# Kernel tuning notes

Hardware: AMD Instinct MI355X
Metric: run time of the kernel (lower is better)

Reference implementation:

```python
import jax, jax.numpy as jnp
import numpy as np

PARENTS = [-1, 0, 0, 0, 1, 2, 3, 4, 5, 6, 7, 8, 9, 9, 9, 12, 13, 14, 16, 17, 18, 19, 20, 21]
K = 24          # num_joints (SMPL kinematic tree)
BONE = 12       # 3x3 rotation (9) + 3 rel offset
FEAT = 64       # local_feature_size
B = 65536       # batch
NIN = BONE + 1 + FEAT  # 77: bone_transform(13) concat parent feature(64)


def setup_inputs() -> dict:
    key = jax.random.key(0)
    ks = jax.random.split(key, 6)
    pose = jax.random.normal(ks[0], (B, K, 3, 3), jnp.float32)
    rel_joints = jax.random.normal(ks[1], (B, K, 3), jnp.float32)
    # proj_bone_prior: Linear(K*BONE -> FEAT)
    Wp = jax.random.normal(ks[2], (K * BONE, FEAT), jnp.float32) * 0.05
    bp = jnp.zeros((FEAT,), jnp.float32)
    # per-joint BoneMLP: Linear(NIN->NIN), ReLU, Linear(NIN->FEAT), ReLU (stacked over K)
    W1 = jax.random.normal(ks[3], (K, NIN, NIN), jnp.float32) * 0.05
    b1 = jnp.zeros((K, NIN), jnp.float32)
    W2 = jax.random.normal(ks[4], (K, NIN, FEAT), jnp.float32) * 0.05
    b2 = jnp.zeros((K, FEAT), jnp.float32)
    return {"pose": pose, "rel_joints": rel_joints, "Wp": Wp, "bp": bp,
            "W1": W1, "b1": b1, "W2": W2, "b2": b2}


def reference(pose, rel_joints, Wp, bp, W1, b1, W2, b2):
    Bn, Kn = rel_joints.shape[0], rel_joints.shape[1]
    bone_lengths = jnp.linalg.norm(rel_joints, axis=-1, keepdims=True)          # B,K,1
    bone_features = jnp.concatenate([pose.reshape(Bn, Kn, 9), rel_joints], -1)  # B,K,12
    root_bone_prior = bone_features.reshape(Bn, -1) @ Wp + bp                   # B,FEAT
    bone_transforms = jnp.concatenate([bone_features, bone_lengths], -1)        # B,K,13
    feats = [None] * Kn
    for i in range(Kn):  # fixed structural loop over kinematic tree (K=24)
        parent = PARENTS[i]
        pf = root_bone_prior if parent == -1 else feats[parent]
        x = jnp.concatenate([bone_transforms[:, i, :], pf], axis=-1)  # B,77
        h = jax.nn.relu(x @ W1[i] + b1[i])
        feats[i] = jax.nn.relu(h @ W2[i] + b2[i])
    return jnp.concatenate(feats, axis=-1)  # B, K*FEAT
```

## Files before the change

### kernel.cpp

```cpp
#include <hip/hip_runtime.h>
#include <hip/hip_bf16.h>
#include <math.h>

typedef __attribute__((ext_vector_type(8))) short short8;
typedef __attribute__((ext_vector_type(4))) float f32x4;

#define NJ 24

#define F1_J   7680
#define F2_OFF (NJ*F1_J)
#define F2_J   6144
#define FP_OFF (F2_OFF + NJ*F2_J)
#define IMG_SHORTS (FP_OFF + 36*512)

#define MFMA(A,B,C) __builtin_amdgcn_mfma_f32_16x16x32_bf16((A),(B),(C),0,0,0)

__constant__ int ORD[24] = {0,1,4,7,10, 2,5,8,11, 3,6,9, 12,15, 13,16,18,20,22, 14,17,19,21,23};
__constant__ int PSL[24] = {2,0,1,1,1,  0,1,1,1,  0,0,0,  0,1,   0,1,1,1,1,    0,0,0,0,0};
__constant__ int SSL[24] = {0,1,1,1,-1, 1,1,1,-1, 0,0,0,  1,-1,  1,1,1,1,-1,   0,0,0,0,-1};

__device__ __forceinline__ short f2bf(float f) {
  union { float f; unsigned u; } v; v.f = f;
  unsigned r = v.u + 0x7FFFu + ((v.u >> 16) & 1u);
  return (short)(r >> 16);
}
__device__ __forceinline__ short sbf(float f) {
  __hip_bfloat16 h = __float2bfloat16(f);
  return *reinterpret_cast<short*>(&h);
}
__device__ __forceinline__ short8 pk8(f32x4 lo, f32x4 hi) {
  union { short8 s; unsigned u[4]; } r;
  asm("v_cvt_pk_bf16_f32 %0, %1, %2" : "=v"(r.u[0]) : "v"(lo[0]), "v"(lo[1]));
  asm("v_cvt_pk_bf16_f32 %0, %1, %2" : "=v"(r.u[1]) : "v"(lo[2]), "v"(lo[3]));
  asm("v_cvt_pk_bf16_f32 %0, %1, %2" : "=v"(r.u[2]) : "v"(hi[0]), "v"(hi[1]));
  asm("v_cvt_pk_bf16_f32 %0, %1, %2" : "=v"(r.u[3]) : "v"(hi[2]), "v"(hi[3]));
  return r.s;
}

__global__ __launch_bounds__(256) void prep_kernel(
    const float* __restrict__ W1, const float* __restrict__ W2,
    const float* __restrict__ Wp, short* __restrict__ img) {
  int t = blockIdx.x * 256 + threadIdx.x;
  if (t >= IMG_SHORTS) return;
  float v = 0.f;
  if (t < F2_OFF) {
    int i = t / F1_J, r = t % F1_J;
    int blk = r >> 9, q = r & 511;
    int ln = q >> 3, e = q & 7;
    int nt = blk / 3, s = blk - nt*3;
    int n  = nt*16 + (ln & 15);
    int kp = s*32 + (ln >> 4)*8 + e;
    if (n < 77) {
      if (kp < 13)                  v = W1[i*5929 + kp*77 + n];
      else if (kp >= 16 && kp < 80) v = W1[i*5929 + (kp-3)*77 + n];
    }
  } else if (t < FP_OFF) {
    int u = t - F2_OFF;
    int i = u / F2_J, r = u % F2_J;
    int blk = r >> 9, q = r & 511;
    int ln = q >> 3, e = q & 7;
    int nt = blk / 3, s = blk - nt*3;
    int n  = nt*16 + (ln & 15);
    int k  = s*32 + (ln >> 4)*8 + e;
    if (k < 77) v = W2[i*4928 + k*64 + n];
  } else {
    int u = t - FP_OFF;
    int blk = u >> 9, q = u & 511;
    int ln = q >> 3, e = q & 7;
    int nt = blk / 9, s = blk - nt*9;
    int n  = nt*16 + (ln & 15);
    int kp = s*32 + (ln >> 4)*8 + e;
    int j, w;
    if (kp < 216) { j = kp / 9;       w = kp % 9; }
    else          { j = (kp-216) / 3; w = 9 + (kp-216) % 3; }
    v = Wp[(j*12 + w)*64 + n];
  }
  img[t] = f2bf(v);
}

struct BT { float p0,p1,p2,p3,p4,p5,p6,p7; };
__device__ __forceinline__ BT bt_load(const float* __restrict__ pose,
                                      const float* __restrict__ rel,
                                      int rw0, int jj, int lane) {
  int r = lane >> 1, q = lane & 1;
  const float* pb = pose + (size_t)(rw0 + r)*216 + (size_t)jj*9;
  const float* rb = rel  + (size_t)(rw0 + r)*72  + (size_t)jj*3;
  BT b;
  if (q == 0) { b.p0=pb[0]; b.p1=pb[1]; b.p2=pb[2]; b.p3=pb[3];
                b.p4=pb[4]; b.p5=pb[5]; b.p6=pb[6]; b.p7=pb[7]; }
  else        { b.p0=pb[8]; b.p1=rb[0]; b.p2=rb[1]; b.p3=rb[2];
                b.p4=0;     b.p5=0;     b.p6=0;     b.p7=0; }
  return b;
}
__device__ __forceinline__ void bt_write(short* btL, BT b, int lane) {
  int r = lane >> 1, q = lane & 1;
  short8 w;
  if (q == 0) {
    w[0]=sbf(b.p0); w[1]=sbf(b.p1); w[2]=sbf(b.p2); w[3]=sbf(b.p3);
    w[4]=sbf(b.p4); w[5]=sbf(b.p5); w[6]=sbf(b.p6); w[7]=sbf(b.p7);
  } else {
    float nv = sqrtf(b.p1*b.p1 + b.p2*b.p2 + b.p3*b.p3);
    w[0]=sbf(b.p0); w[1]=sbf(b.p1); w[2]=sbf(b.p2); w[3]=sbf(b.p3);
    w[4]=sbf(nv);   w[5]=0; w[6]=0; w[7]=0;
  }
  *(short8*)(btL + r*24 + q*8) = w;
}

#define ISSUE_W1(JN) do { \
  unsigned long long _b = img_u + (unsigned long long)(JN)*15360ull; \
  asm volatile( \
    "global_load_dwordx4 %0, %15, %16\n"  "global_load_dwordx4 %1, %15, %16 offset:1024\n" \
    "global_load_dwordx4 %2, %15, %16 offset:2048\n" "global_load_dwordx4 %3, %15, %16 offset:3072\n" \
    "global_load_dwordx4 %4, %15, %17\n"  "global_load_dwordx4 %5, %15, %17 offset:1024\n" \
    "global_load_dwordx4 %6, %15, %17 offset:2048\n" "global_load_dwordx4 %7, %15, %17 offset:3072\n" \
    "global_load_dwordx4 %8, %15, %18\n"  "global_load_dwordx4 %9, %15, %18 offset:1024\n" \
    "global_load_dwordx4 %10, %15, %18 offset:2048\n" "global_load_dwordx4 %11, %15, %18 offset:3072\n" \
    "global_load_dwordx4 %12, %15, %19\n" "global_load_dwordx4 %13, %15, %19 offset:1024\n" \
    "global_load_dwordx4 %14, %15, %19 offset:2048\n" \
    : "=v"(fw1[0]),"=v"(fw1[1]),"=v"(fw1[2]),"=v"(fw1[3]),"=v"(fw1[4]), \
      "=v"(fw1[5]),"=v"(fw1[6]),"=v"(fw1[7]),"=v"(fw1[8]),"=v"(fw1[9]), \
      "=v"(fw1[10]),"=v"(fw1[11]),"=v"(fw1[12]),"=v"(fw1[13]),"=v"(fw1[14]) \
    : "v"(voff), "s"(_b), "s"(_b+4096ull), "s"(_b+8192ull), "s"(_b+12288ull) \
    : "memory"); \
} while(0)

#define ISSUE_W2(J) do { \
  unsigned long long _b = img_u + 368640ull + (unsigned long long)(J)*12288ull; \
  asm volatile( \
    "global_load_dwordx4 %0, %12, %13\n"  "global_load_dwordx4 %1, %12, %13 offset:1024\n" \
    "global_load_dwordx4 %2, %12, %13 offset:2048\n" "global_load_dwordx4 %3, %12, %13 offset:3072\n" \
    "global_load_dwordx4 %4, %12, %14\n"  "global_load_dwordx4 %5, %12, %14 offset:1024\n" \
    "global_load_dwordx4 %6, %12, %14 offset:2048\n" "global_load_dwordx4 %7, %12, %14 offset:3072\n" \
    "global_load_dwordx4 %8, %12, %15\n"  "global_load_dwordx4 %9, %12, %15 offset:1024\n" \
    "global_load_dwordx4 %10, %12, %15 offset:2048\n" "global_load_dwordx4 %11, %12, %15 offset:3072\n" \
    : "=v"(fw2[0]),"=v"(fw2[1]),"=v"(fw2[2]),"=v"(fw2[3]),"=v"(fw2[4]),"=v"(fw2[5]), \
      "=v"(fw2[6]),"=v"(fw2[7]),"=v"(fw2[8]),"=v"(fw2[9]),"=v"(fw2[10]),"=v"(fw2[11]) \
    : "v"(voff), "s"(_b), "s"(_b+4096ull), "s"(_b+8192ull) \
    : "memory"); \
} while(0)

#define WAITV(N) do { asm volatile("s_waitcnt vmcnt(" #N ")" ::: "memory"); \
                      __builtin_amdgcn_sched_barrier(0); } while(0)

__global__ __launch_bounds__(256, 2) void enc_kernel(
    const float* __restrict__ pose, const float* __restrict__ rel,
    const float* __restrict__ bp,  const float* __restrict__ b1,
    const float* __restrict__ b2,  const short* __restrict__ img,
    float* __restrict__ out) {
  __shared__ __align__(16) short lds[4*9984];

  const int tid  = threadIdx.x;
  const int lane = tid & 63;
  const int wv   = tid >> 6;
  short* myl   = lds + wv*9984;
  short* featL = myl;
  short* hL    = myl + 6528;
  short* btL   = myl + 9216;

  const int cl  = lane & 15;
  const int g   = lane >> 4;
  const int rw0 = blockIdx.x*128 + wv*32;
  const short8 zz = {0,0,0,0,0,0,0,0};
  const unsigned long long img_u = (unsigned long long)img;
  const unsigned voff = (unsigned)lane << 4;

  short8 fw1[15], fw2[12];

  BT nb = bt_load(pose, rel, rw0, 0, lane);
  ISSUE_W1(0);

  f32x4 racc[2][4] = {};
  {
    const float* pr0 = pose + (size_t)(rw0 + cl)*216;
    const float* rr0 = rel  + (size_t)(rw0 + cl)*72;
    const float* pr1 = pose + (size_t)(rw0 + 16 + cl)*216;
    const float* rr1 = rel  + (size_t)(rw0 + 16 + cl)*72;
    const short8* fpg = (const short8*)(img + FP_OFF) + lane;
    short8 av0[9], av1[9];
#pragma unroll
    for (int s = 0; s < 9; ++s) {
      int k0 = s*32 + g*8;
      const float* s0 = (k0 < 216) ? (pr0 + k0) : (rr0 + (k0 - 216));
      const float* s1 = (k0 < 216) ? (pr1 + k0) : (rr1 + (k0 - 216));
      av0[s] = pk8(*(const f32x4*)s0, *(const f32x4*)(s0 + 4));
      av1[s] = pk8(*(const f32x4*)s1, *(const f32x4*)(s1 + 4));
    }
#pragma unroll
    for (int nt = 0; nt < 4; ++nt) {
      short8 fwp[9];
#pragma unroll
      for (int s = 0; s < 9; ++s) fwp[s] = fpg[(nt*9 + s)*64];
#pragma unroll
      for (int s = 0; s < 9; ++s) {
        racc[0][nt] = MFMA(av0[s], fwp[s], racc[0][nt]);
        racc[1][nt] = MFMA(av1[s], fwp[s], racc[1][nt]);
      }
    }
  }
#pragma unroll
  for (int nt = 0; nt < 4; ++nt) {
    int n = nt*16 + cl;
    float bias = bp[n];
#pragma unroll
    for (int m = 0; m < 2; ++m)
#pragma unroll
      for (int r4 = 0; r4 < 4; ++r4)
        featL[2*2176 + (m*16 + g*4 + r4)*68 + n] = sbf(racc[m][nt][r4] + bias);
  }
  bt_write(btL, nb, lane);

#pragma unroll 1
  for (int p = 0; p < NJ; ++p) {
    const int j  = ORD[p];
    const int ps = PSL[p];
    const int ss = SSL[p];
    const int jn = (p < NJ-1) ? ORD[p+1] : 0;

    if (p < NJ-1) nb = bt_load(pose, rel, rw0, jn, lane);
    float bl1[5], bl2[4];
#pragma unroll
    for (int nt = 0; nt < 5; ++nt) {
      int n = nt*16 + cl;
      bl1[nt] = (n < 77) ? b1[j*77 + n] : 0.f;
    }
#pragma unroll
    for (int nt = 0; nt < 4; ++nt) bl2[nt] = b2[j*64 + nt*16 + cl];

    const short* fb0 = featL + ps*2176 + cl*68;
    const short* fb1 = featL + ps*2176 + (16 + cl)*68;
    short8 a0[2], a1[2], a2[2];
    a0[0] = (g < 2) ? *(const short8*)(btL + cl*24 + g*8)
                    : *(const short8*)(fb0 + (g-2)*8);
    a0[1] = (g < 2) ? *(const short8*)(btL + (16+cl)*24 + g*8)
                    : *(const short8*)(fb1 + (g-2)*8);
    a1[0] = *(const short8*)(fb0 + 16 + g*8);
    a1[1] = *(const short8*)(fb1 + 16 + g*8);
    a2[0] = (g < 2) ? *(const short8*)(fb0 + 48 + g*8) : zz;
    a2[1] = (g < 2) ? *(const short8*)(fb1 + 48 + g*8) : zz;

    ISSUE_W2(j);
    WAITV(12);

#pragma unroll
    for (int nt = 0; nt < 5; ++nt) {
      f32x4 c0 = {0,0,0,0}, c1 = {0,0,0,0};
      c0 = MFMA(a0[0], fw1[nt*3+0], c0);  c1 = MFMA(a0[1], fw1[nt*3+0], c1);
      c0 = MFMA(a1[0], fw1[nt*3+1], c0);  c1 = MFMA(a1[1], fw1[nt*3+1], c1);
      c0 = MFMA(a2[0], fw1[nt*3+2], c0);  c1 = MFMA(a2[1], fw1[nt*3+2], c1);
      int n = nt*16 + cl;
#pragma unroll
      for (int r4 = 0; r4 < 4; ++r4) {
        hL[(g*4 + r4)*84 + n]      = sbf(fmaxf(c0[r4] + bl1[nt], 0.f));
        hL[(16 + g*4 + r4)*84 + n] = sbf(fmaxf(c1[r4] + bl1[nt], 0.f));
      }
    }
    short8 h0[2], h1[2], h2[2];
#pragma unroll
    for (int m = 0; m < 2; ++m) {
      const short* hb = hL + (m*16 + cl)*84;
      h0[m] = *(const short8*)(hb + g*8);
      h1[m] = *(const short8*)(hb + 32 + g*8);
      h2[m] = (g < 2) ? *(const short8*)(hb + 64 + g*8) : zz;
    }
    if (p < NJ-1) bt_write(btL, nb, lane);

    if (p < NJ-1) { ISSUE_W1(jn); WAITV(15); }
    else          { WAITV(0); }

#pragma unroll
    for (int nt = 0; nt < 4; ++nt) {
      f32x4 c0 = {0,0,0,0}, c1 = {0,0,0,0};
      c0 = MFMA(h0[0], fw2[nt*3+0], c0);  c1 = MFMA(h0[1], fw2[nt*3+0], c1);
      c0 = MFMA(h1[0], fw2[nt*3+1], c0);  c1 = MFMA(h1[1], fw2[nt*3+1], c1);
      c0 = MFMA(h2[0], fw2[nt*3+2], c0);  c1 = MFMA(h2[1], fw2[nt*3+2], c1);
      int n = nt*16 + cl;
#pragma unroll
      for (int m = 0; m < 2; ++m) {
        f32x4& cc = m ? c1 : c0;
        float* outb = out + (size_t)(rw0 + m*16 + g*4)*1536 + (size_t)j*64;
#pragma unroll
        for (int r4 = 0; r4 < 4; ++r4) {
          float v = fmaxf(cc[r4] + bl2[nt], 0.f);
          __builtin_nontemporal_store(v, &outb[(size_t)r4*1536 + n]);
          if (ss >= 0) featL[ss*2176 + (m*16 + g*4 + r4)*68 + n] = sbf(v);
        }
      }
    }
  }
}

extern "C" void kernel_launch(void* const* d_in, const int* in_sizes, int n_in,
                              void* d_out, int out_size, void* d_ws, size_t ws_size,
                              hipStream_t stream) {
  const float* pose = (const float*)d_in[0];
  const float* rel  = (const float*)d_in[1];
  const float* Wp   = (const float*)d_in[2];
  const float* bp   = (const float*)d_in[3];
  const float* W1   = (const float*)d_in[4];
  const float* b1   = (const float*)d_in[5];
  const float* W2   = (const float*)d_in[6];
  const float* b2   = (const float*)d_in[7];
  float* outp = (float*)d_out;
  short* img  = (short*)d_ws;
  const int Bn = in_sizes[0] / 216;
  prep_kernel<<<(IMG_SHORTS + 255)/256, 256, 0, stream>>>(W1, W2, Wp, img);
  enc_kernel<<<Bn/128, 256, 0, stream>>>(pose, rel, bp, b1, b2, img, outp);
}
```

Before: 155.3 us.

## Fold biases into GEMM weights via constant-one column and asm-prefetch bone inputs

```diff
diff --git a/kernel.cpp b/kernel.cpp
--- a/kernel.cpp
+++ b/kernel.cpp
@@ -39,7 +39,8 @@
 
 __global__ __launch_bounds__(256) void prep_kernel(
     const float* __restrict__ W1, const float* __restrict__ W2,
-    const float* __restrict__ Wp, short* __restrict__ img) {
+    const float* __restrict__ Wp, const float* __restrict__ b1,
+    const float* __restrict__ b2, short* __restrict__ img) {
   int t = blockIdx.x * 256 + threadIdx.x;
   if (t >= IMG_SHORTS) return;
   float v = 0.f;
@@ -50,7 +51,9 @@
     int nt = blk / 3, s = blk - nt*3;
     int n  = nt*16 + (ln & 15);
     int kp = s*32 + (ln >> 4)*8 + e;
-    if (n < 77) {
+    if (kp == 13) {
+      v = (n < 77) ? b1[i*77 + n] : (n == 77 ? 1.f : 0.f);
+    } else if (n < 77) {
       if (kp < 13)                  v = W1[i*5929 + kp*77 + n];
       else if (kp >= 16 && kp < 80) v = W1[i*5929 + (kp-3)*77 + n];
     }
@@ -62,7 +65,8 @@
     int nt = blk / 3, s = blk - nt*3;
     int n  = nt*16 + (ln & 15);
     int k  = s*32 + (ln >> 4)*8 + e;
-    if (k < 77) v = W2[i*4928 + k*64 + n];
+    if (k < 77)       v = W2[i*4928 + k*64 + n];
+    else if (k == 77) v = b2[i*64 + n];
   } else {
     int u = t - FP_OFF;
     int blk = u >> 9, q = u & 511;
@@ -78,34 +82,6 @@
   img[t] = f2bf(v);
 }
 
-struct BT { float p0,p1,p2,p3,p4,p5,p6,p7; };
-__device__ __forceinline__ BT bt_load(const float* __restrict__ pose,
-                                      const float* __restrict__ rel,
-                                      int rw0, int jj, int lane) {
-  int r = lane >> 1, q = lane & 1;
-  const float* pb = pose + (size_t)(rw0 + r)*216 + (size_t)jj*9;
-  const float* rb = rel  + (size_t)(rw0 + r)*72  + (size_t)jj*3;
-  BT b;
-  if (q == 0) { b.p0=pb[0]; b.p1=pb[1]; b.p2=pb[2]; b.p3=pb[3];
-                b.p4=pb[4]; b.p5=pb[5]; b.p6=pb[6]; b.p7=pb[7]; }
-  else        { b.p0=pb[8]; b.p1=rb[0]; b.p2=rb[1]; b.p3=rb[2];
-                b.p4=0;     b.p5=0;     b.p6=0;     b.p7=0; }
-  return b;
-}
-__device__ __forceinline__ void bt_write(short* btL, BT b, int lane) {
-  int r = lane >> 1, q = lane & 1;
-  short8 w;
-  if (q == 0) {
-    w[0]=sbf(b.p0); w[1]=sbf(b.p1); w[2]=sbf(b.p2); w[3]=sbf(b.p3);
-    w[4]=sbf(b.p4); w[5]=sbf(b.p5); w[6]=sbf(b.p6); w[7]=sbf(b.p7);
-  } else {
-    float nv = sqrtf(b.p1*b.p1 + b.p2*b.p2 + b.p3*b.p3);
-    w[0]=sbf(b.p0); w[1]=sbf(b.p1); w[2]=sbf(b.p2); w[3]=sbf(b.p3);
-    w[4]=sbf(nv);   w[5]=0; w[6]=0; w[7]=0;
-  }
-  *(short8*)(btL + r*24 + q*8) = w;
-}
-
 #define ISSUE_W1(JN) do { \
   unsigned long long _b = img_u + (unsigned long long)(JN)*15360ull; \
   asm volatile( \
@@ -117,25 +93,35 @@
     "global_load_dwordx4 %10, %15, %18 offset:2048\n" "global_load_dwordx4 %11, %15, %18 offset:3072\n" \
     "global_load_dwordx4 %12, %15, %19\n" "global_load_dwordx4 %13, %15, %19 offset:1024\n" \
     "global_load_dwordx4 %14, %15, %19 offset:2048\n" \
-    : "=v"(fw1[0]),"=v"(fw1[1]),"=v"(fw1[2]),"=v"(fw1[3]),"=v"(fw1[4]), \
-      "=v"(fw1[5]),"=v"(fw1[6]),"=v"(fw1[7]),"=v"(fw1[8]),"=v"(fw1[9]), \
-      "=v"(fw1[10]),"=v"(fw1[11]),"=v"(fw1[12]),"=v"(fw1[13]),"=v"(fw1[14]) \
+    : "=&v"(fw1[0]),"=&v"(fw1[1]),"=&v"(fw1[2]),"=&v"(fw1[3]),"=&v"(fw1[4]), \
+      "=&v"(fw1[5]),"=&v"(fw1[6]),"=&v"(fw1[7]),"=&v"(fw1[8]),"=&v"(fw1[9]), \
+      "=&v"(fw1[10]),"=&v"(fw1[11]),"=&v"(fw1[12]),"=&v"(fw1[13]),"=&v"(fw1[14]) \
     : "v"(voff), "s"(_b), "s"(_b+4096ull), "s"(_b+8192ull), "s"(_b+12288ull) \
     : "memory"); \
 } while(0)
 
-#define ISSUE_W2(J) do { \
+#define ISSUE_BTW2(J) do { \
   unsigned long long _b = img_u + 368640ull + (unsigned long long)(J)*12288ull; \
   asm volatile( \
-    "global_load_dwordx4 %0, %12, %13\n"  "global_load_dwordx4 %1, %12, %13 offset:1024\n" \
-    "global_load_dwordx4 %2, %12, %13 offset:2048\n" "global_load_dwordx4 %3, %12, %13 offset:3072\n" \
-    "global_load_dwordx4 %4, %12, %14\n"  "global_load_dwordx4 %5, %12, %14 offset:1024\n" \
-    "global_load_dwordx4 %6, %12, %14 offset:2048\n" "global_load_dwordx4 %7, %12, %14 offset:3072\n" \
-    "global_load_dwordx4 %8, %12, %15\n"  "global_load_dwordx4 %9, %12, %15 offset:1024\n" \
-    "global_load_dwordx4 %10, %12, %15 offset:2048\n" "global_load_dwordx4 %11, %12, %15 offset:3072\n" \
-    : "=v"(fw2[0]),"=v"(fw2[1]),"=v"(fw2[2]),"=v"(fw2[3]),"=v"(fw2[4]),"=v"(fw2[5]), \
-      "=v"(fw2[6]),"=v"(fw2[7]),"=v"(fw2[8]),"=v"(fw2[9]),"=v"(fw2[10]),"=v"(fw2[11]) \
-    : "v"(voff), "s"(_b), "s"(_b+4096ull), "s"(_b+8192ull) \
+    "global_load_dword %0, %20, off\n" \
+    "global_load_dword %1, %20, off offset:4\n" \
+    "global_load_dword %2, %20, off offset:8\n" \
+    "global_load_dword %3, %20, off offset:12\n" \
+    "global_load_dword %4, %21, %22\n" \
+    "global_load_dword %5, %21, %22 offset:4\n" \
+    "global_load_dword %6, %21, %22 offset:8\n" \
+    "global_load_dword %7, %21, %22 offset:12\n" \
+    "global_load_dwordx4 %8, %23, %24\n"  "global_load_dwordx4 %9, %23, %24 offset:1024\n" \
+    "global_load_dwordx4 %10, %23, %24 offset:2048\n" "global_load_dwordx4 %11, %23, %24 offset:3072\n" \
+    "global_load_dwordx4 %12, %23, %25\n" "global_load_dwordx4 %13, %23, %25 offset:1024\n" \
+    "global_load_dwordx4 %14, %23, %25 offset:2048\n" "global_load_dwordx4 %15, %23, %25 offset:3072\n" \
+    "global_load_dwordx4 %16, %23, %26\n" "global_load_dwordx4 %17, %23, %26 offset:1024\n" \
+    "global_load_dwordx4 %18, %23, %26 offset:2048\n" "global_load_dwordx4 %19, %23, %26 offset:3072\n" \
+    : "=&v"(d0),"=&v"(d1),"=&v"(d2),"=&v"(d3),"=&v"(d4),"=&v"(d5),"=&v"(d6),"=&v"(d7), \
+      "=&v"(fw2[0]),"=&v"(fw2[1]),"=&v"(fw2[2]),"=&v"(fw2[3]),"=&v"(fw2[4]),"=&v"(fw2[5]), \
+      "=&v"(fw2[6]),"=&v"(fw2[7]),"=&v"(fw2[8]),"=&v"(fw2[9]),"=&v"(fw2[10]),"=&v"(fw2[11]) \
+    : "v"(aA), "v"(vB), "s"(pose_u), "v"(voff), \
+      "s"(_b), "s"(_b+4096ull), "s"(_b+8192ull) \
     : "memory"); \
 } while(0)
 
@@ -144,30 +130,47 @@
 
 __global__ __launch_bounds__(256, 2) void enc_kernel(
     const float* __restrict__ pose, const float* __restrict__ rel,
-    const float* __restrict__ bp,  const float* __restrict__ b1,
-    const float* __restrict__ b2,  const short* __restrict__ img,
+    const float* __restrict__ bp,  const short* __restrict__ img,
     float* __restrict__ out) {
-  __shared__ __align__(16) short lds[4*9984];
+  __shared__ __align__(16) short lds[4*10240];
 
   const int tid  = threadIdx.x;
   const int lane = tid & 63;
   const int wv   = tid >> 6;
-  short* myl   = lds + wv*9984;
+  short* myl   = lds + wv*10240;
   short* featL = myl;
-  short* hL    = myl + 6528;
-  short* btL   = myl + 9216;
+  short* hL    = myl + 6912;
+  short* btL   = myl + 9472;
 
   const int cl  = lane & 15;
   const int g   = lane >> 4;
   const int rw0 = blockIdx.x*128 + wv*32;
   const short8 zz = {0,0,0,0,0,0,0,0};
-  const unsigned long long img_u = (unsigned long long)img;
+  const unsigned long long img_u  = (unsigned long long)img;
+  const unsigned long long pose_u = (unsigned long long)pose;
+  const unsigned long long rel_u  = (unsigned long long)rel;
   const unsigned voff = (unsigned)lane << 4;
+  const int btr = lane >> 1, btq = lane & 1;
+  const unsigned btProw = (unsigned)((rw0 + btr)*864);
+  const unsigned btRrow = (unsigned)((rw0 + btr)*288);
 
   short8 fw1[15], fw2[12];
-
-  BT nb = bt_load(pose, rel, rw0, 0, lane);
-  ISSUE_W1(0);
+  float d0, d1, d2, d3, d4, d5, d6, d7;
+
+  {
+    const float* pb = pose + (size_t)(rw0 + btr)*216;
+    const float* rb = rel  + (size_t)(rw0 + btr)*72;
+    short8 w;
+    if (btq == 0) {
+      w = pk8(*(const f32x4*)pb, *(const f32x4*)(pb + 4));
+    } else {
+      float r0 = rb[0], r1 = rb[1], r2 = rb[2];
+      float nv = sqrtf(r0*r0 + r1*r1 + r2*r2);
+      w[0]=sbf(pb[8]); w[1]=sbf(r0); w[2]=sbf(r1); w[3]=sbf(r2);
+      w[4]=sbf(nv); w[5]=(short)0x3F80; w[6]=0; w[7]=0;
+    }
+    *(short8*)(btL + btr*24 + btq*8) = w;
+  }
 
   f32x4 racc[2][4] = {};
   {
@@ -205,9 +208,10 @@
     for (int m = 0; m < 2; ++m)
 #pragma unroll
       for (int r4 = 0; r4 < 4; ++r4)
-        featL[2*2176 + (m*16 + g*4 + r4)*68 + n] = sbf(racc[m][nt][r4] + bias);
-  }
-  bt_write(btL, nb, lane);
+        featL[2*2304 + (m*16 + g*4 + r4)*72 + n] = sbf(racc[m][nt][r4] + bias);
+  }
+
+  ISSUE_W1(0);
 
 #pragma unroll 1
   for (int p = 0; p < NJ; ++p) {
@@ -216,18 +220,8 @@
     const int ss = SSL[p];
     const int jn = (p < NJ-1) ? ORD[p+1] : 0;
 
-    if (p < NJ-1) nb = bt_load(pose, rel, rw0, jn, lane);
-    float bl1[5], bl2[4];
-#pragma unroll
-    for (int nt = 0; nt < 5; ++nt) {
-      int n = nt*16 + cl;
-      bl1[nt] = (n < 77) ? b1[j*77 + n] : 0.f;
-    }
-#pragma unroll
-    for (int nt = 0; nt < 4; ++nt) bl2[nt] = b2[j*64 + nt*16 + cl];
-
-    const short* fb0 = featL + ps*2176 + cl*68;
-    const short* fb1 = featL + ps*2176 + (16 + cl)*68;
+    const short* fb0 = featL + ps*2304 + cl*72;
+    const short* fb1 = featL + ps*2304 + (16 + cl)*72;
     short8 a0[2], a1[2], a2[2];
     a0[0] = (g < 2) ? *(const short8*)(btL + cl*24 + g*8)
                     : *(const short8*)(fb0 + (g-2)*8);
@@ -238,8 +232,13 @@
     a2[0] = (g < 2) ? *(const short8*)(fb0 + 48 + g*8) : zz;
     a2[1] = (g < 2) ? *(const short8*)(fb1 + 48 + g*8) : zz;
 
-    ISSUE_W2(j);
-    WAITV(12);
+    const unsigned long long aA =
+        btq ? (rel_u  + btRrow + (unsigned)(jn ? jn*12 - 4 : 0))
+            : (pose_u + btProw + (unsigned)(jn*36));
+    const unsigned vB = btProw + (unsigned)(jn*36) + (btq ? 20u : 16u);
+    ISSUE_BTW2(j);
+
+    if (p == 0) { WAITV(20); } else { WAITV(52); }
 
 #pragma unroll
     for (int nt = 0; nt < 5; ++nt) {
@@ -250,22 +249,35 @@
       int n = nt*16 + cl;
 #pragma unroll
       for (int r4 = 0; r4 < 4; ++r4) {
-        hL[(g*4 + r4)*84 + n]      = sbf(fmaxf(c0[r4] + bl1[nt], 0.f));
-        hL[(16 + g*4 + r4)*84 + n] = sbf(fmaxf(c1[r4] + bl1[nt], 0.f));
+        hL[(g*4 + r4)*80 + n]      = sbf(fmaxf(c0[r4], 0.f));
+        hL[(16 + g*4 + r4)*80 + n] = sbf(fmaxf(c1[r4], 0.f));
       }
     }
     short8 h0[2], h1[2], h2[2];
 #pragma unroll
     for (int m = 0; m < 2; ++m) {
-      const short* hb = hL + (m*16 + cl)*84;
+      const short* hb = hL + (m*16 + cl)*80;
       h0[m] = *(const short8*)(hb + g*8);
       h1[m] = *(const short8*)(hb + 32 + g*8);
       h2[m] = (g < 2) ? *(const short8*)(hb + 64 + g*8) : zz;
     }
-    if (p < NJ-1) bt_write(btL, nb, lane);
-
-    if (p < NJ-1) { ISSUE_W1(jn); WAITV(15); }
-    else          { WAITV(0); }
+
+    ISSUE_W1(jn);
+    WAITV(15);
+
+    {
+      f32x4 lo = {d0, d1, d2, d3}, hi = {d4, d5, d6, d7};
+      short8 wA = pk8(lo, hi);
+      float r0 = jn ? d1 : d0;
+      float r1 = jn ? d2 : d1;
+      float r2 = jn ? d3 : d2;
+      float nv = sqrtf(r0*r0 + r1*r1 + r2*r2);
+      short8 wB;
+      wB[0]=sbf(d7);   wB[1]=sbf(r0); wB[2]=sbf(r1); wB[3]=sbf(r2);
+      wB[4]=sbf(nv); wB[5]=(short)0x3F80; wB[6]=0; wB[7]=0;
+      short8 w = btq ? wB : wA;
+      *(short8*)(btL + btr*24 + btq*8) = w;
+    }
 
 #pragma unroll
     for (int nt = 0; nt < 4; ++nt) {
@@ -280,9 +292,9 @@
         float* outb = out + (size_t)(rw0 + m*16 + g*4)*1536 + (size_t)j*64;
 #pragma unroll
         for (int r4 = 0; r4 < 4; ++r4) {
-          float v = fmaxf(cc[r4] + bl2[nt], 0.f);
+          float v = fmaxf(cc[r4], 0.f);
           __builtin_nontemporal_store(v, &outb[(size_t)r4*1536 + n]);
-          if (ss >= 0) featL[ss*2176 + (m*16 + g*4 + r4)*68 + n] = sbf(v);
+          if (ss >= 0) featL[ss*2304 + (m*16 + g*4 + r4)*72 + n] = sbf(v);
         }
       }
     }
@@ -303,6 +315,6 @@
   float* outp = (float*)d_out;
   short* img  = (short*)d_ws;
   const int Bn = in_sizes[0] / 216;
-  prep_kernel<<<(IMG_SHORTS + 255)/256, 256, 0, stream>>>(W1, W2, Wp, img);
-  enc_kernel<<<Bn/128, 256, 0, stream>>>(pose, rel, bp, b1, b2, img, outp);
-}
+  prep_kernel<<<(IMG_SHORTS + 255)/256, 256, 0, stream>>>(W1, W2, Wp, b1, b2, img);
+  enc_kernel<<<Bn/128, 256, 0, stream>>>(pose, rel, bp, img, outp);
+}
```

Result: no change. 154.4 us (-0.6%).
